# Kernel optimization log

Hardware: AMD Instinct MI355X
Metric: run time of the kernel (lower is better)

Reference implementation:

```python
import math
import jax, jax.numpy as jnp
import numpy as np

B, T, D, H, E, K = 2, 2048, 1024, 16, 8, 2
HD = D // H                      # head_dim = 64
CAP = math.ceil(1.25 * B * T / E)  # capacity per expert = 640
NEG = -1e9


def setup_inputs() -> dict:
    key = jax.random.key(0)
    ks = jax.random.split(key, 8)
    s = 0.02
    return {
        "x": jax.random.normal(ks[0], (B, T, D), jnp.float32),
        "ln1_g": jnp.ones((D,), jnp.float32),
        "ln1_b": jnp.zeros((D,), jnp.float32),
        "w_qkv": jax.random.normal(ks[1], (3 * D, D), jnp.float32) * s,
        "w_proj": jax.random.normal(ks[2], (D, D), jnp.float32) * s,
        "ln2_g": jnp.ones((D,), jnp.float32),
        "ln2_b": jnp.zeros((D,), jnp.float32),
        "w_gate": jax.random.normal(ks[3], (E, D), jnp.float32) * s,
        "w1": jax.random.normal(ks[4], (E, D, 4 * D), jnp.float32) * s,
        "b1": jnp.zeros((E, 4 * D), jnp.float32),
        "w2": jax.random.normal(ks[5], (E, 4 * D, D), jnp.float32) * s,
        "b2": jnp.zeros((E, D), jnp.float32),
    }


def _layernorm(x, g, b, eps=1e-5):
    m = x.mean(-1, keepdims=True)
    v = ((x - m) ** 2).mean(-1, keepdims=True)
    return (x - m) * jax.lax.rsqrt(v + eps) * g + b


def _rope(q, k):
    # q,k: [B,T,H,HD]; rotate-half RoPE with half_dim = HD//2 frequencies
    half = HD // 2
    pos = jnp.arange(T, dtype=jnp.float32)[:, None]
    inv_freq = 1.0 / (10000.0 ** (jnp.arange(0, HD, 2, dtype=jnp.float32) / HD))
    ang = pos * inv_freq                              # [T, half]
    sin = jnp.sin(ang)[None, :, None, :]
    cos = jnp.cos(ang)[None, :, None, :]

    def rot(t):
        t1, t2 = t[..., :half], t[..., half:]
        return jnp.concatenate([t1 * cos - t2 * sin, t1 * sin + t2 * cos], -1)

    return rot(q), rot(k)


def _attention(x, w_qkv, w_proj):
    qkv = (x @ w_qkv.T).reshape(B, T, H, 3 * HD)
    q, k, v = jnp.split(qkv, 3, axis=-1)              # each [B,T,H,HD]
    q, k = _rope(q, k)
    scores = jnp.einsum('bqhd,bkhd->bhqk', q, k) / math.sqrt(HD)
    causal = jnp.tril(jnp.ones((T, T), bool))
    scores = jnp.where(causal, scores, NEG)
    probs = jax.nn.softmax(scores, axis=-1)
    out = jnp.einsum('bhqk,bkhd->bqhd', probs, v).reshape(B, T, D)
    return out @ w_proj.T


def _sparse_moe(x2d, w_gate, w1, b1, w2, b2):
    # x2d: [N, D] flattened tokens. Eval mode: no noise, no dropout.
    N = x2d.shape[0]
    gates = jax.nn.softmax((x2d @ w_gate.T).astype(jnp.float32), axis=-1)  # [N,E]
    gate_vals, idx = jax.lax.top_k(gates, K)          # [N,K]
    gate_vals = gate_vals.astype(x2d.dtype)

    # Capacity enforcement: token order position within each expert
    mask = jnp.zeros((N, E), bool).at[jnp.arange(N)[:, None], idx].set(True)
    pos = jnp.cumsum(mask.astype(jnp.int32), axis=0) * mask - 1   # [N,E]
    keep = (pos < CAP) & mask
    slot = jnp.take_along_axis(pos, idx, axis=1)      # [N,K]
    kept = jnp.take_along_axis(keep, idx, axis=1)     # [N,K] bool

    # Dispatch: dropped tokens go to pad slot CAP (masked out at combine)
    slot_w = jnp.where(kept, slot, CAP).reshape(-1)   # [N*K]
    e_flat = idx.reshape(-1)                          # [N*K]
    xk = jnp.broadcast_to(x2d[:, None, :], (N, K, D)).reshape(-1, D)
    xk = xk * kept.reshape(-1, 1)
    buf = jnp.zeros((E, CAP + 1, D), x2d.dtype).at[e_flat, slot_w].set(xk)

    # Grouped expert MLP (GELU exact, matching nn.GELU default)
    h = jax.nn.gelu(jnp.einsum('ecd,edf->ecf', buf, w1) + b1[:, None, :],
                    approximate=False)
    out = jnp.einsum('ecf,efd->ecd', h, w2) + b2[:, None, :]

    # Combine: gather each token's expert output, weight by gate, mask drops
    y = out[e_flat, slot_w].reshape(N, K, D) * (gate_vals * kept)[..., None]
    return y.sum(axis=1)


def reference(x, ln1_g, ln1_b, w_qkv, w_proj, ln2_g, ln2_b,
              w_gate, w1, b1, w2, b2):
    h = x + _attention(_layernorm(x, ln1_g, ln1_b), w_qkv, w_proj)
    moe_in = _layernorm(h, ln2_g, ln2_b)
    moe_out = _sparse_moe(moe_in.reshape(B * T, D), w_gate, w1, b1, w2, b2)
    return h + moe_out.reshape(B, T, D)
```

## Files before the change

kernel.cpp:

```cpp
#include <hip/hip_runtime.h>
#include <hip/hip_bf16.h>

typedef __bf16 bf16;
typedef __attribute__((ext_vector_type(8))) __bf16 bf16x8;
typedef __attribute__((ext_vector_type(4))) __bf16 bf16x4;
typedef __attribute__((ext_vector_type(4))) float f32x4;
typedef __attribute__((ext_vector_type(16))) float f32x16;

#define NB 2
#define NT 2048
#define ND 1024
#define NH 16
#define HD_ 64
#define NE 8
#define NCAP 640
#define NTOK 4096
#define NDFF 4096

static __device__ __forceinline__ f32x4 mfma16(bf16x8 a, bf16x8 b, f32x4 c) {
  return __builtin_amdgcn_mfma_f32_16x16x32_bf16(a, b, c, 0, 0, 0);
}
static __device__ __forceinline__ f32x16 mfma32(bf16x8 a, bf16x8 b, f32x16 c) {
  return __builtin_amdgcn_mfma_f32_32x32x16_bf16(a, b, c, 0, 0, 0);
}
static __device__ __forceinline__ unsigned pk2(float a, float b) {
  union { __bf16 h[2]; unsigned u; } z;
  z.h[0] = (__bf16)a; z.h[1] = (__bf16)b;
  return z.u;
}
static __device__ __forceinline__ void gload_lds16(const bf16* g, bf16* l) {
  __builtin_amdgcn_global_load_lds(
      (const __attribute__((address_space(1))) unsigned int*)g,
      (__attribute__((address_space(3))) unsigned int*)l, 16, 0, 0);
}

__global__ __launch_bounds__(256) void cvt_k(const float* __restrict__ in,
                                             bf16* __restrict__ out, int n4) {
  int i = blockIdx.x * 256 + threadIdx.x;
  int stride = gridDim.x * 256;
  for (; i < n4; i += stride) {
    f32x4 v = ((const f32x4*)in)[i];
    bf16x4 o;
    o[0] = (bf16)v[0]; o[1] = (bf16)v[1]; o[2] = (bf16)v[2]; o[3] = (bf16)v[3];
    ((bf16x4*)out)[i] = o;
  }
}

__global__ __launch_bounds__(256) void transpose_k(const float* __restrict__ in,
                                                   bf16* __restrict__ out, int R, int C) {
  __shared__ float tile[64][65];
  const size_t zoff = (size_t)blockIdx.z * R * C;
  in += zoff; out += zoff;
  const int c0 = blockIdx.x * 64, r0 = blockIdx.y * 64;
  const int tx = threadIdx.x & 15, ty = threadIdx.x >> 4;
#pragma unroll
  for (int i = 0; i < 4; i++) {
    const int r = i * 16 + ty;
    f32x4 v = *(const f32x4*)(in + (size_t)(r0 + r) * C + c0 + tx * 4);
    *(f32x4*)&tile[r][tx * 4] = v;
  }
  __syncthreads();
#pragma unroll
  for (int i = 0; i < 4; i++) {
    const int rr = i * 16 + ty;
    bf16x4 o;
#pragma unroll
    for (int j = 0; j < 4; j++) o[j] = (bf16)tile[tx * 4 + j][rr];
    *(bf16x4*)(out + (size_t)(c0 + rr) * R + r0 + tx * 4) = o;
  }
}

__global__ __launch_bounds__(256) void transpose_v_k(const bf16* __restrict__ v,
                                                     bf16* __restrict__ vT) {
  __shared__ bf16 tile[32][33];
  int bh = blockIdx.z;
  const bf16* in = v + (size_t)bh * NT * HD_;
  bf16* out = vT + (size_t)bh * HD_ * NT;
  int t0 = blockIdx.x * 32, d0 = blockIdx.y * 32;
  int tx = threadIdx.x, ty = threadIdx.y;
#pragma unroll
  for (int i = 0; i < 4; i++)
    tile[ty + i * 8][tx] = in[(size_t)(t0 + ty + i * 8) * HD_ + d0 + tx];
  __syncthreads();
#pragma unroll
  for (int i = 0; i < 4; i++)
    out[(size_t)(d0 + ty + i * 8) * NT + t0 + tx] = tile[tx][ty + i * 8];
}

__global__ void rope_tab_k(float* __restrict__ tab) {
  int t = blockIdx.x, i = threadIdx.x;
  float inv = powf(10000.f, -(float)(2 * i) * (1.f / 64.f));
  float ang = (float)t * inv;
  float s, c;
  sincosf(ang, &s, &c);
  tab[(t * 32 + i) * 2] = s;
  tab[(t * 32 + i) * 2 + 1] = c;
}

template <bool BF16OUT>
__global__ __launch_bounds__(256) void ln_k(const float* __restrict__ in,
                                            const float* __restrict__ g,
                                            const float* __restrict__ bb,
                                            bf16* __restrict__ outb,
                                            float* __restrict__ outf) {
  const int row = blockIdx.x;
  const float* xr = in + (size_t)row * ND;
  const int tid = threadIdx.x, lane = tid & 63, wid = tid >> 6;
  f32x4 v = ((const f32x4*)xr)[tid];
  float s = v[0] + v[1] + v[2] + v[3];
  float sq = v[0] * v[0] + v[1] * v[1] + v[2] * v[2] + v[3] * v[3];
#pragma unroll
  for (int m = 1; m < 64; m <<= 1) {
    s += __shfl_xor(s, m, 64);
    sq += __shfl_xor(sq, m, 64);
  }
  __shared__ float red[8];
  if (lane == 0) { red[wid] = s; red[4 + wid] = sq; }
  __syncthreads();
  s = red[0] + red[1] + red[2] + red[3];
  sq = red[4] + red[5] + red[6] + red[7];
  float mean = s * (1.f / 1024.f);
  float var = sq * (1.f / 1024.f) - mean * mean;
  float rs = rsqrtf(var + 1e-5f);
#pragma unroll
  for (int c = 0; c < 4; c++) {
    int col = tid * 4 + c;
    float y = (v[c] - mean) * rs * g[col] + bb[col];
    if constexpr (BF16OUT) outb[(size_t)row * ND + col] = (bf16)y;
    else outf[(size_t)row * ND + col] = y;
  }
}

#define EPI_SPLIT_QKV 0
#define EPI_ADD_X 1
#define EPI_BIAS_GELU 2
#define EPI_STORE 3

template <int EPI, int STAGE>
__global__ __launch_bounds__(256) void gemm_bt_k(
    const bf16* __restrict__ A, const bf16* __restrict__ Bw,
    const int M, const int N, const int K,
    const size_t zA, const size_t zB, const size_t zOut, const size_t zBias,
    const float* __restrict__ bias, const float* __restrict__ Xadd,
    void* __restrict__ Out, bf16* __restrict__ k_out, bf16* __restrict__ v_out) {
  const int z = blockIdx.z;
  const int m0 = blockIdx.y * 128, n0 = blockIdx.x * 128;
  const int tid = threadIdx.x, lane = tid & 63, wid = tid >> 6;
  const int wm = (wid >> 1) * 64, wn = (wid & 1) * 64;
  const int l15 = lane & 15, ksl = lane >> 4;
  const int nst = K / 64;
  constexpr int LDB = (STAGE == 1) ? 72 : 64;
  __shared__ __align__(16) bf16 As[128 * LDB];
  __shared__ __align__(16) bf16 Bs[128 * LDB];
  f32x4 acc[4][4];
#pragma unroll
  for (int i = 0; i < 4; i++)
#pragma unroll
    for (int j = 0; j < 4; j++) acc[i][j] = (f32x4){0.f, 0.f, 0.f, 0.f};

  if constexpr (STAGE == 0) {
    const int lr = lane >> 3, lc = (lane & 7) * 8;
    const bf16* Ag = A + zA * z + (size_t)(m0 + wid * 32 + lr) * K + lc;
    const bf16* Bg = Bw + zB * z + (size_t)(n0 + wid * 32 + lr) * K + lc;
    for (int s = 0; s < nst; ++s) {
      __syncthreads();
#pragma unroll
      for (int it = 0; it < 4; it++) {
        gload_lds16(Ag + (size_t)(it * 8) * K + s * 64, &As[(wid * 32 + it * 8) * 64]);
        gload_lds16(Bg + (size_t)(it * 8) * K + s * 64, &Bs[(wid * 32 + it * 8) * 64]);
      }
      __syncthreads();
#pragma unroll
      for (int kk = 0; kk < 2; kk++) {
        bf16x8 af[4], bfr[4];
        const int ko = kk * 32 + ksl * 8;
#pragma unroll
        for (int i = 0; i < 4; i++)
          af[i] = *(const bf16x8*)&As[(wm + i * 16 + l15) * 64 + ko];
#pragma unroll
        for (int j = 0; j < 4; j++)
          bfr[j] = *(const bf16x8*)&Bs[(wn + j * 16 + l15) * 64 + ko];
#pragma unroll
        for (int i = 0; i < 4; i++)
#pragma unroll
          for (int j = 0; j < 4; j++)
            acc[i][j] = mfma16(af[i], bfr[j], acc[i][j]);
      }
    }
  } else {
    const int sr = tid >> 3, sc = (tid & 7) * 8;
    const bf16* Ag = A + zA * z + (size_t)(m0 + sr) * K + sc;
    const bf16* Bg = Bw + zB * z + (size_t)(n0 + sr) * K + sc;
    bf16x8 av[4], bv[4];
#pragma unroll
    for (int it = 0; it < 4; it++) {
      av[it] = *(const bf16x8*)(Ag + (size_t)(it * 32) * K);
      bv[it] = *(const bf16x8*)(Bg + (size_t)(it * 32) * K);
    }
    for (int s = 0; s < nst; ++s) {
      __syncthreads();
#pragma unroll
      for (int it = 0; it < 4; it++) {
        *(bf16x8*)&As[(sr + it * 32) * LDB + sc] = av[it];
        *(bf16x8*)&Bs[(sr + it * 32) * LDB + sc] = bv[it];
      }
      __syncthreads();
      if (s + 1 < nst) {
#pragma unroll
        for (int it = 0; it < 4; it++) {
          av[it] = *(const bf16x8*)(Ag + (size_t)(it * 32) * K + (s + 1) * 64);
          bv[it] = *(const bf16x8*)(Bg + (size_t)(it * 32) * K + (s + 1) * 64);
        }
      }
#pragma unroll
      for (int kk = 0; kk < 2; kk++) {
        bf16x8 af[4], bfr[4];
        const int ko = kk * 32 + ksl * 8;
#pragma unroll
        for (int i = 0; i < 4; i++)
          af[i] = *(const bf16x8*)&As[(wm + i * 16 + l15) * LDB + ko];
#pragma unroll
        for (int j = 0; j < 4; j++)
          bfr[j] = *(const bf16x8*)&Bs[(wn + j * 16 + l15) * LDB + ko];
#pragma unroll
        for (int i = 0; i < 4; i++)
#pragma unroll
          for (int j = 0; j < 4; j++)
            acc[i][j] = mfma16(af[i], bfr[j], acc[i][j]);
      }
    }
  }

#pragma unroll
  for (int i = 0; i < 4; i++) {
#pragma unroll
    for (int j = 0; j < 4; j++) {
      const int mb = m0 + wm + i * 16 + ksl * 4;
      const int nc = n0 + wn + j * 16 + l15;
#pragma unroll
      for (int r = 0; r < 4; r++) {
        const int mr = mb + r;
        float vacc = acc[i][j][r];
        if constexpr (EPI == EPI_SPLIT_QKV) {
          const int h = nc / 192;
          const int rr = nc - h * 192;
          const int which = rr >> 6;
          const int d = rr & 63;
          const int b = mr >> 11, t = mr & 2047;
          bf16* dst = (which == 0) ? (bf16*)Out : (which == 1 ? k_out : v_out);
          dst[(((size_t)(b * NH + h)) * NT + t) * HD_ + d] = (bf16)vacc;
        } else if constexpr (EPI == EPI_ADD_X) {
          ((float*)Out)[(size_t)mr * N + nc] = vacc + Xadd[(size_t)mr * N + nc];
        } else if constexpr (EPI == EPI_BIAS_GELU) {
          float x = vacc + bias[zBias * z + nc];
          float gl = 0.5f * x * (1.f + erff(x * 0.70710678118654752f));
          ((bf16*)Out)[zOut * z + (size_t)mr * N + nc] = (bf16)gl;
        } else {
          ((bf16*)Out)[zOut * z + (size_t)mr * N + nc] = (bf16)vacc;
        }
      }
    }
  }
}

__global__ __launch_bounds__(256) void rope_k(bf16* __restrict__ q, bf16* __restrict__ k,
                                              const float* __restrict__ tab) {
  const int bh = blockIdx.y;
  const int t = blockIdx.x * 4 + (threadIdx.x >> 6);
  const int d = threadIdx.x & 63;
  const size_t row = ((size_t)bh * NT + t) * HD_;
  const int i = d & 31;
  const float sn = tab[(t * 32 + i) * 2], cs = tab[(t * 32 + i) * 2 + 1];
  {
    float a = (float)q[row + d];
    float b2 = (float)q[row + (d ^ 32)];
    float o = (d < 32) ? (a * cs - b2 * sn) : (b2 * sn + a * cs);
    q[row + d] = (bf16)(o * 0.18033688011112042f);
  }
  {
    float a = (float)k[row + d];
    float b2 = (float)k[row + (d ^ 32)];
    float o = (d < 32) ? (a * cs - b2 * sn) : (b2 * sn + a * cs);
    k[row + d] = (bf16)o;
  }
}

__global__ __launch_bounds__(256) void attn_k(const bf16* __restrict__ q,
                                              const bf16* __restrict__ k,
                                              const bf16* __restrict__ vT,
                                              bf16* __restrict__ attn_out) {
  __shared__ __align__(16) bf16 Kt[64 * 64];
  __shared__ __align__(16) bf16 Vt[64 * 64];
  const int bid = blockIdx.x;
  const int bh = bid & 31;
  const int ti = (bid >> 5) & 7;
  const int qt = (bid >> 8) ? (15 - ti) : ti;
  const int q0 = qt * 128;
  const int tid = threadIdx.x, lane = tid & 63, wid = tid >> 6;
  const int l31 = lane & 31, hi = lane >> 5;
  const int q0w = q0 + wid * 32;
  const int qrow = q0w + l31;
  const size_t base = (size_t)bh * (NT * HD_);
  const size_t baseT = (size_t)bh * (HD_ * NT);

  bf16x8 qf[4];
#pragma unroll
  for (int ks = 0; ks < 4; ks++)
    qf[ks] = *(const bf16x8*)(q + base + (size_t)qrow * HD_ + ks * 16 + hi * 8);

  f32x16 ot0, ot1;
#pragma unroll
  for (int r = 0; r < 16; r++) { ot0[r] = 0.f; ot1[r] = 0.f; }
  float m2 = -1e30f, l = 0.f;

  const int ntiles = qt * 2 + 2;
  const int swz = (l31 & 7);
  const int strow = tid >> 3, stc = tid & 7;
  const int cw0 = ((stc ^ (strow & 7)) * 8);
  bf16x8 kr[2], vr[2];
#pragma unroll
  for (int rr = 0; rr < 2; rr++) {
    kr[rr] = *(const bf16x8*)(k + base + (size_t)(strow + rr * 32) * HD_ + stc * 8);
    vr[rr] = *(const bf16x8*)(vT + baseT + (size_t)(strow + rr * 32) * NT + stc * 8);
  }

  for (int t = 0; t < ntiles; t++) {
    const int kv0 = t * 64;
    __syncthreads();
#pragma unroll
    for (int rr = 0; rr < 2; rr++) {
      *(bf16x8*)&Kt[(strow + rr * 32) * 64 + cw0] = kr[rr];
      *(bf16x8*)&Vt[(strow + rr * 32) * 64 + cw0] = vr[rr];
    }
    __syncthreads();
    if (t + 1 < ntiles) {
      const int kn = kv0 + 64;
#pragma unroll
      for (int rr = 0; rr < 2; rr++) {
        kr[rr] = *(const bf16x8*)(k + base + (size_t)(kn + strow + rr * 32) * HD_ + stc * 8);
        vr[rr] = *(const bf16x8*)(vT + baseT + (size_t)(strow + rr * 32) * NT + kn + stc * 8);
      }
    }
    if (kv0 > q0w + 31) continue;

    f32x16 s0, s1;
#pragma unroll
    for (int r = 0; r < 16; r++) { s0[r] = 0.f; s1[r] = 0.f; }
#pragma unroll
    for (int ks = 0; ks < 4; ks++) {
      const int cw = (((ks * 2 + hi) ^ swz) * 8);
      bf16x8 ka0 = *(const bf16x8*)&Kt[l31 * 64 + cw];
      bf16x8 ka1 = *(const bf16x8*)&Kt[(l31 + 32) * 64 + cw];
      s0 = mfma32(ka0, qf[ks], s0);
      s1 = mfma32(ka1, qf[ks], s1);
    }

    float p[32];
#pragma unroll
    for (int r = 0; r < 16; r++) { p[r] = s0[r]; p[16 + r] = s1[r]; }
    if (kv0 + 63 > q0w) {
#pragma unroll
      for (int sub = 0; sub < 2; sub++)
#pragma unroll
        for (int r = 0; r < 16; r++) {
          int kvg = kv0 + sub * 32 + (r & 3) + 8 * (r >> 2) + 4 * hi;
          if (kvg > qrow) p[sub * 16 + r] = -1e30f;
        }
    }
    float tm = p[0];
#pragma unroll
    for (int r = 1; r < 32; r++) tm = fmaxf(tm, p[r]);
    tm = fmaxf(tm, __shfl_xor(tm, 32, 64));
    if (!__all(tm <= m2 + 8.f)) {
      float mn = fmaxf(m2, tm);
      float sf = exp2f(m2 - mn);
      m2 = mn;
      l *= sf;
#pragma unroll
      for (int r = 0; r < 16; r++) { ot0[r] *= sf; ot1[r] *= sf; }
    }
    float ts = 0.f;
#pragma unroll
    for (int r = 0; r < 32; r++) { p[r] = exp2f(p[r] - m2); ts += p[r]; }
    ts += __shfl_xor(ts, 32, 64);
    l += ts;

#pragma unroll
    for (int ks = 0; ks < 4; ks++) {
      const int i0 = (ks >> 1) * 16 + (ks & 1) * 8;
      unsigned Aw = pk2(p[i0 + 0], p[i0 + 1]);
      unsigned Bw = pk2(p[i0 + 2], p[i0 + 3]);
      unsigned Cw = pk2(p[i0 + 4], p[i0 + 5]);
      unsigned Dw = pk2(p[i0 + 6], p[i0 + 7]);
      unsigned xA = (unsigned)__shfl_xor((int)Aw, 32, 64);
      unsigned xB = (unsigned)__shfl_xor((int)Bw, 32, 64);
      unsigned xC = (unsigned)__shfl_xor((int)Cw, 32, 64);
      unsigned xD = (unsigned)__shfl_xor((int)Dw, 32, 64);
      union { unsigned u[4]; bf16x8 v; } pa;
      pa.u[0] = hi ? xC : Aw;
      pa.u[1] = hi ? xD : Bw;
      pa.u[2] = hi ? Cw : xA;
      pa.u[3] = hi ? Dw : xB;
      const int cw = (((ks * 2 + hi) ^ swz) * 8);
      bf16x8 va0 = *(const bf16x8*)&Vt[l31 * 64 + cw];
      bf16x8 va1 = *(const bf16x8*)&Vt[(l31 + 32) * 64 + cw];
      ot0 = mfma32(va0, pa.v, ot0);
      ot1 = mfma32(va1, pa.v, ot1);
    }
  }

  const int b = bh >> 4, h = bh & 15;
  const float inv = 1.f / l;
  const size_t orow = ((size_t)(b * NT + qrow)) * ND + h * 64;
#pragma unroll
  for (int g = 0; g < 4; g++) {
    bf16x4 w0, w1;
#pragma unroll
    for (int c = 0; c < 4; c++) {
      w0[c] = (bf16)(ot0[g * 4 + c] * inv);
      w1[c] = (bf16)(ot1[g * 4 + c] * inv);
    }
    *(bf16x4*)(attn_out + orow + g * 8 + 4 * hi) = w0;
    *(bf16x4*)(attn_out + orow + 32 + g * 8 + 4 * hi) = w1;
  }
}

__global__ __launch_bounds__(256) void gate_k(const float* __restrict__ moe_in,
                                              const float* __restrict__ w_gate,
                                              int* __restrict__ idx, float* __restrict__ gv) {
  __shared__ float wg[8 * 1024];
  for (int i = threadIdx.x; i < 8192; i += 256) wg[i] = w_gate[i];
  __syncthreads();
  const int lane = threadIdx.x & 63, wid = threadIdx.x >> 6;
  for (int tt = 0; tt < 4; tt++) {
    const int n = blockIdx.x * 16 + wid * 4 + tt;
    const float* xr = moe_in + (size_t)n * ND;
    float a[8];
#pragma unroll
    for (int e = 0; e < 8; e++) a[e] = 0.f;
    for (int d0 = lane * 4; d0 < 1024; d0 += 256) {
      f32x4 xv = *(const f32x4*)(xr + d0);
#pragma unroll
      for (int e = 0; e < 8; e++) {
        const float* wr = &wg[e * 1024 + d0];
        a[e] += xv[0] * wr[0] + xv[1] * wr[1] + xv[2] * wr[2] + xv[3] * wr[3];
      }
    }
#pragma unroll
    for (int e = 0; e < 8; e++)
#pragma unroll
      for (int m = 1; m < 64; m <<= 1) a[e] += __shfl_xor(a[e], m, 64);
    if (lane == 0) {
      float mx = a[0];
#pragma unroll
      for (int e = 1; e < 8; e++) mx = fmaxf(mx, a[e]);
      float p[8], se = 0.f;
#pragma unroll
      for (int e = 0; e < 8; e++) { p[e] = expf(a[e] - mx); se += p[e]; }
      float inv = 1.f / se;
#pragma unroll
      for (int e = 0; e < 8; e++) p[e] *= inv;
      int i1 = 0; float v1 = p[0];
#pragma unroll
      for (int e = 1; e < 8; e++) if (p[e] > v1) { v1 = p[e]; i1 = e; }
      int i2 = -1; float v2 = -1.f;
#pragma unroll
      for (int e = 0; e < 8; e++) if (e != i1 && p[e] > v2) { v2 = p[e]; i2 = e; }
      idx[n * 2] = i1; idx[n * 2 + 1] = i2;
      gv[n * 2] = v1; gv[n * 2 + 1] = v2;
    }
  }
}

__global__ void scan_k(const int* __restrict__ idx, int* __restrict__ slot,
                       int* __restrict__ kept) {
  const int lane = threadIdx.x;
  int base[8];
#pragma unroll
  for (int e = 0; e < 8; e++) base[e] = 0;
  const unsigned long long lm = (lane == 63) ? ~0ull : ((1ull << (lane + 1)) - 1);
  for (int c = 0; c < 64; c++) {
    const int n = c * 64 + lane;
    const int e0 = idx[n * 2], e1 = idx[n * 2 + 1];
    int s0 = 0, s1 = 0;
#pragma unroll
    for (int e = 0; e < 8; e++) {
      unsigned long long m0 = __ballot(e0 == e);
      unsigned long long m1 = __ballot(e1 == e);
      unsigned long long m = m0 | m1;
      int pref = __popcll(m & lm);
      if (e0 == e) s0 = base[e] + pref - 1;
      if (e1 == e) s1 = base[e] + pref - 1;
      base[e] += __popcll(m);
    }
    slot[n * 2] = s0; slot[n * 2 + 1] = s1;
    kept[n * 2] = (s0 < NCAP) ? 1 : 0;
    kept[n * 2 + 1] = (s1 < NCAP) ? 1 : 0;
  }
}

__global__ __launch_bounds__(64) void scatter_k(const float* __restrict__ moe_in,
                                                const int* __restrict__ idx,
                                                const int* __restrict__ slot,
                                                const int* __restrict__ kept,
                                                bf16* __restrict__ buf) {
  const int a = blockIdx.x;
  if (!kept[a]) return;
  const int n = a >> 1;
  const int e = idx[a], s = slot[a];
  const float* src = moe_in + (size_t)n * ND;
  bf16* dst = buf + ((size_t)e * NCAP + s) * ND;
  for (int c = threadIdx.x * 4; c < 1024; c += 256) {
    f32x4 v = *(const f32x4*)(src + c);
    bf16x4 o;
    o[0] = (bf16)v[0]; o[1] = (bf16)v[1]; o[2] = (bf16)v[2]; o[3] = (bf16)v[3];
    *(bf16x4*)(dst + c) = o;
  }
}

__global__ __launch_bounds__(256) void gather_k(const float* __restrict__ h,
                                                const bf16* __restrict__ eout,
                                                const int* __restrict__ idx,
                                                const int* __restrict__ slot,
                                                const int* __restrict__ kept,
                                                const float* __restrict__ gv,
                                                const float* __restrict__ b2,
                                                float* __restrict__ out) {
  const int n = blockIdx.x;
  const int k0 = kept[n * 2], k1 = kept[n * 2 + 1];
  const int i0 = idx[n * 2], i1 = idx[n * 2 + 1];
  const float g0 = k0 ? gv[n * 2] : 0.f;
  const float g1 = k1 ? gv[n * 2 + 1] : 0.f;
  const size_t r0 = k0 ? ((size_t)i0 * NCAP + slot[n * 2]) * ND : 0;
  const size_t r1 = k1 ? ((size_t)i1 * NCAP + slot[n * 2 + 1]) * ND : 0;
  const int c = threadIdx.x * 4;
  f32x4 o = *(const f32x4*)(h + (size_t)n * ND + c);
  if (k0) {
    bf16x4 e = *(const bf16x4*)(eout + r0 + c);
    f32x4 bb = *(const f32x4*)(b2 + i0 * ND + c);
#pragma unroll
    for (int cc = 0; cc < 4; cc++) o[cc] += g0 * ((float)e[cc] + bb[cc]);
  }
  if (k1) {
    bf16x4 e = *(const bf16x4*)(eout + r1 + c);
    f32x4 bb = *(const f32x4*)(b2 + i1 * ND + c);
#pragma unroll
    for (int cc = 0; cc < 4; cc++) o[cc] += g1 * ((float)e[cc] + bb[cc]);
  }
  *(f32x4*)(out + (size_t)n * ND + c) = o;
}

extern "C" void kernel_launch(void* const* d_in, const int* in_sizes, int n_in,
                              void* d_out, int out_size, void* d_ws, size_t ws_size,
                              hipStream_t stream) {
  (void)in_sizes; (void)n_in; (void)out_size;
  const float* x      = (const float*)d_in[0];
  const float* ln1_g  = (const float*)d_in[1];
  const float* ln1_b  = (const float*)d_in[2];
  const float* w_qkv  = (const float*)d_in[3];
  const float* w_proj = (const float*)d_in[4];
  const float* ln2_g  = (const float*)d_in[5];
  const float* ln2_b  = (const float*)d_in[6];
  const float* w_gate = (const float*)d_in[7];
  const float* w1     = (const float*)d_in[8];
  const float* b1     = (const float*)d_in[9];
  const float* w2     = (const float*)d_in[10];
  const float* b2     = (const float*)d_in[11];
  float* out = (float*)d_out;

  char* ws = (char*)d_ws;
  size_t off = 0;
  auto alloc = [&](size_t bytes) -> char* {
    char* p = ws + off;
    off += (bytes + 255) & ~(size_t)255;
    return p;
  };
  bf16* w1t    = (bf16*)alloc((size_t)NE * NDFF * ND * 2);
  bf16* w2t    = (bf16*)alloc((size_t)NE * ND * NDFF * 2);
  bf16* wqkvb  = (bf16*)alloc((size_t)3 * ND * ND * 2);
  bf16* wprojb = (bf16*)alloc((size_t)ND * ND * 2);
  float* hbufr = (float*)alloc((size_t)NTOK * ND * 4);
  float* moein = (float*)alloc((size_t)NTOK * ND * 4);
  float* ropet = (float*)alloc((size_t)NT * 32 * 2 * 4);
  int*   idx   = (int*)alloc((size_t)NTOK * 2 * 4);
  int*   slot  = (int*)alloc((size_t)NTOK * 2 * 4);
  int*   kept  = (int*)alloc((size_t)NTOK * 2 * 4);
  float* gv    = (float*)alloc((size_t)NTOK * 2 * 4);
  char*  S     = alloc((size_t)62914560);
  if (off > ws_size) return;

  const size_t MB8 = (size_t)8388608;
  bf16* xn    = (bf16*)(S);
  bf16* qp    = (bf16*)(S + MB8);
  bf16* kp    = (bf16*)(S + 2 * MB8);
  bf16* vp    = (bf16*)(S + 3 * MB8);
  bf16* attnp = (bf16*)(S + 4 * MB8);
  bf16* vTp   = (bf16*)(S);
  bf16* hbuf  = (bf16*)(S);
  bf16* buf   = (bf16*)(S + (size_t)41943040);
  bf16* eout  = (bf16*)(S + (size_t)52428800);

  dim3 tb(32, 8);
  cvt_k<<<2048, 256, 0, stream>>>(w_qkv, wqkvb, 3 * ND * ND / 4);
  cvt_k<<<1024, 256, 0, stream>>>(w_proj, wprojb, ND * ND / 4);
  transpose_k<<<dim3(NDFF / 64, ND / 64, NE), 256, 0, stream>>>(w1, w1t, ND, NDFF);
  transpose_k<<<dim3(ND / 64, NDFF / 64, NE), 256, 0, stream>>>(w2, w2t, NDFF, ND);
  rope_tab_k<<<NT, 32, 0, stream>>>(ropet);
  ln_k<true><<<NTOK, 256, 0, stream>>>(x, ln1_g, ln1_b, xn, nullptr);
  gemm_bt_k<EPI_SPLIT_QKV, 0><<<dim3(3 * ND / 128, NTOK / 128, 1), 256, 0, stream>>>(
      xn, wqkvb, NTOK, 3 * ND, ND, 0, 0, 0, 0, nullptr, nullptr, qp, kp, vp);
  transpose_v_k<<<dim3(NT / 32, HD_ / 32, NB * NH), tb, 0, stream>>>(vp, vTp);
  rope_k<<<dim3(NT / 4, NB * NH), 256, 0, stream>>>(qp, kp, ropet);
  attn_k<<<512, 256, 0, stream>>>(qp, kp, vTp, attnp);
  gemm_bt_k<EPI_ADD_X, 1><<<dim3(ND / 128, NTOK / 128, 1), 256, 0, stream>>>(
      attnp, wprojb, NTOK, ND, ND, 0, 0, 0, 0, nullptr, x, hbufr, nullptr, nullptr);
  ln_k<false><<<NTOK, 256, 0, stream>>>(hbufr, ln2_g, ln2_b, nullptr, moein);
  gate_k<<<NTOK / 16, 256, 0, stream>>>(moein, w_gate, idx, gv);
  scan_k<<<1, 64, 0, stream>>>(idx, slot, kept);
  scatter_k<<<NTOK * 2, 64, 0, stream>>>(moein, idx, slot, kept, buf);
  gemm_bt_k<EPI_BIAS_GELU, 0><<<dim3(NDFF / 128, NCAP / 128, NE), 256, 0, stream>>>(
      buf, w1t, NCAP, NDFF, ND, (size_t)NCAP * ND, (size_t)NDFF * ND,
      (size_t)NCAP * NDFF, NDFF, b1, nullptr, hbuf, nullptr, nullptr);
  gemm_bt_k<EPI_STORE, 1><<<dim3(ND / 128, NCAP / 128, NE), 256, 0, stream>>>(
      hbuf, w2t, NCAP, ND, NDFF, (size_t)NCAP * NDFF, (size_t)ND * NDFF,
      (size_t)NCAP * ND, 0, nullptr, nullptr, eout, nullptr, nullptr);
  gather_k<<<NTOK, 256, 0, stream>>>(hbufr, eout, idx, slot, kept, gv, b2, out);
}
```

Measured before the change: 459.1 us.

## Split-K the expert down-projection with fp32 atomics and use sigmoid GELU approximation

The second expert GEMM (K=4096) now splits K four ways across the grid z dimension. Each split accumulates into a zeroed fp32 output through atomic adds, which raises the block count from 320 to 1280 for better CU occupancy. The gather kernel now reads that fp32 output. The exact erf GELU is replaced by a sigmoid-based approximation, x*sigmoid(poly(x)), which is cheaper but deviates slightly from exact GELU. LDS padding is also disabled for that GEMM. The change adds a memset, atomic traffic and a larger fp32 intermediate.

```diff
diff --git a/kernel.cpp b/kernel.cpp
--- a/kernel.cpp
+++ b/kernel.cpp
@@ -134,22 +134,26 @@
 #define EPI_SPLIT_QKV 0
 #define EPI_ADD_X 1
 #define EPI_BIAS_GELU 2
-#define EPI_STORE 3
-
-template <int EPI, int STAGE>
+#define EPI_ATOMIC 3
+
+template <int EPI, int STAGE, bool PAD>
 __global__ __launch_bounds__(256) void gemm_bt_k(
     const bf16* __restrict__ A, const bf16* __restrict__ Bw,
-    const int M, const int N, const int K,
+    const int M, const int N, const int K, const int nsplit,
     const size_t zA, const size_t zB, const size_t zOut, const size_t zBias,
     const float* __restrict__ bias, const float* __restrict__ Xadd,
     void* __restrict__ Out, bf16* __restrict__ k_out, bf16* __restrict__ v_out) {
   const int z = blockIdx.z;
+  const int ze = z / nsplit;
+  const int kc = z - ze * nsplit;
+  const int klen = K / nsplit;
+  const int kb = kc * klen;
+  const int nst = klen / 64;
   const int m0 = blockIdx.y * 128, n0 = blockIdx.x * 128;
   const int tid = threadIdx.x, lane = tid & 63, wid = tid >> 6;
   const int wm = (wid >> 1) * 64, wn = (wid & 1) * 64;
   const int l15 = lane & 15, ksl = lane >> 4;
-  const int nst = K / 64;
-  constexpr int LDB = (STAGE == 1) ? 72 : 64;
+  constexpr int LDB = (STAGE == 1 && PAD) ? 72 : 64;
   __shared__ __align__(16) bf16 As[128 * LDB];
   __shared__ __align__(16) bf16 Bs[128 * LDB];
   f32x4 acc[4][4];
@@ -160,8 +164,8 @@
 
   if constexpr (STAGE == 0) {
     const int lr = lane >> 3, lc = (lane & 7) * 8;
-    const bf16* Ag = A + zA * z + (size_t)(m0 + wid * 32 + lr) * K + lc;
-    const bf16* Bg = Bw + zB * z + (size_t)(n0 + wid * 32 + lr) * K + lc;
+    const bf16* Ag = A + zA * ze + (size_t)(m0 + wid * 32 + lr) * K + kb + lc;
+    const bf16* Bg = Bw + zB * ze + (size_t)(n0 + wid * 32 + lr) * K + kb + lc;
     for (int s = 0; s < nst; ++s) {
       __syncthreads();
 #pragma unroll
@@ -189,8 +193,8 @@
     }
   } else {
     const int sr = tid >> 3, sc = (tid & 7) * 8;
-    const bf16* Ag = A + zA * z + (size_t)(m0 + sr) * K + sc;
-    const bf16* Bg = Bw + zB * z + (size_t)(n0 + sr) * K + sc;
+    const bf16* Ag = A + zA * ze + (size_t)(m0 + sr) * K + kb + sc;
+    const bf16* Bg = Bw + zB * ze + (size_t)(n0 + sr) * K + kb + sc;
     bf16x8 av[4], bv[4];
 #pragma unroll
     for (int it = 0; it < 4; it++) {
@@ -252,11 +256,12 @@
         } else if constexpr (EPI == EPI_ADD_X) {
           ((float*)Out)[(size_t)mr * N + nc] = vacc + Xadd[(size_t)mr * N + nc];
         } else if constexpr (EPI == EPI_BIAS_GELU) {
-          float x = vacc + bias[zBias * z + nc];
-          float gl = 0.5f * x * (1.f + erff(x * 0.70710678118654752f));
-          ((bf16*)Out)[zOut * z + (size_t)mr * N + nc] = (bf16)gl;
+          float x = vacc + bias[zBias * ze + nc];
+          float u2 = x * (2.3020882f + 0.10294772f * x * x);
+          float gl = x / (1.f + exp2f(-u2));
+          ((bf16*)Out)[zOut * ze + (size_t)mr * N + nc] = (bf16)gl;
         } else {
-          ((bf16*)Out)[zOut * z + (size_t)mr * N + nc] = (bf16)vacc;
+          unsafeAtomicAdd(&((float*)Out)[zOut * ze + (size_t)mr * N + nc], vacc);
         }
       }
     }
@@ -519,7 +524,7 @@
 }
 
 __global__ __launch_bounds__(256) void gather_k(const float* __restrict__ h,
-                                                const bf16* __restrict__ eout,
+                                                const float* __restrict__ eout,
                                                 const int* __restrict__ idx,
                                                 const int* __restrict__ slot,
                                                 const int* __restrict__ kept,
@@ -536,16 +541,16 @@
   const int c = threadIdx.x * 4;
   f32x4 o = *(const f32x4*)(h + (size_t)n * ND + c);
   if (k0) {
-    bf16x4 e = *(const bf16x4*)(eout + r0 + c);
+    f32x4 e = *(const f32x4*)(eout + r0 + c);
     f32x4 bb = *(const f32x4*)(b2 + i0 * ND + c);
 #pragma unroll
-    for (int cc = 0; cc < 4; cc++) o[cc] += g0 * ((float)e[cc] + bb[cc]);
+    for (int cc = 0; cc < 4; cc++) o[cc] += g0 * (e[cc] + bb[cc]);
   }
   if (k1) {
-    bf16x4 e = *(const bf16x4*)(eout + r1 + c);
+    f32x4 e = *(const f32x4*)(eout + r1 + c);
     f32x4 bb = *(const f32x4*)(b2 + i1 * ND + c);
 #pragma unroll
-    for (int cc = 0; cc < 4; cc++) o[cc] += g1 * ((float)e[cc] + bb[cc]);
+    for (int cc = 0; cc < 4; cc++) o[cc] += g1 * (e[cc] + bb[cc]);
   }
   *(f32x4*)(out + (size_t)n * ND + c) = o;
 }
@@ -596,9 +601,9 @@
   bf16* vp    = (bf16*)(S + 3 * MB8);
   bf16* attnp = (bf16*)(S + 4 * MB8);
   bf16* vTp   = (bf16*)(S);
-  bf16* hbuf  = (bf16*)(S);
-  bf16* buf   = (bf16*)(S + (size_t)41943040);
-  bf16* eout  = (bf16*)(S + (size_t)52428800);
+  bf16*  hbuf  = (bf16*)(S);
+  bf16*  buf   = (bf16*)(S + (size_t)41943040);
+  float* eoutf = (float*)(S + (size_t)41943040);
 
   dim3 tb(32, 8);
   cvt_k<<<2048, 256, 0, stream>>>(w_qkv, wqkvb, 3 * ND * ND / 4);
@@ -607,22 +612,23 @@
   transpose_k<<<dim3(ND / 64, NDFF / 64, NE), 256, 0, stream>>>(w2, w2t, NDFF, ND);
   rope_tab_k<<<NT, 32, 0, stream>>>(ropet);
   ln_k<true><<<NTOK, 256, 0, stream>>>(x, ln1_g, ln1_b, xn, nullptr);
-  gemm_bt_k<EPI_SPLIT_QKV, 0><<<dim3(3 * ND / 128, NTOK / 128, 1), 256, 0, stream>>>(
-      xn, wqkvb, NTOK, 3 * ND, ND, 0, 0, 0, 0, nullptr, nullptr, qp, kp, vp);
+  gemm_bt_k<EPI_SPLIT_QKV, 0, false><<<dim3(3 * ND / 128, NTOK / 128, 1), 256, 0, stream>>>(
+      xn, wqkvb, NTOK, 3 * ND, ND, 1, 0, 0, 0, 0, nullptr, nullptr, qp, kp, vp);
   transpose_v_k<<<dim3(NT / 32, HD_ / 32, NB * NH), tb, 0, stream>>>(vp, vTp);
   rope_k<<<dim3(NT / 4, NB * NH), 256, 0, stream>>>(qp, kp, ropet);
   attn_k<<<512, 256, 0, stream>>>(qp, kp, vTp, attnp);
-  gemm_bt_k<EPI_ADD_X, 1><<<dim3(ND / 128, NTOK / 128, 1), 256, 0, stream>>>(
-      attnp, wprojb, NTOK, ND, ND, 0, 0, 0, 0, nullptr, x, hbufr, nullptr, nullptr);
+  gemm_bt_k<EPI_ADD_X, 1, true><<<dim3(ND / 128, NTOK / 128, 1), 256, 0, stream>>>(
+      attnp, wprojb, NTOK, ND, ND, 1, 0, 0, 0, 0, nullptr, x, hbufr, nullptr, nullptr);
   ln_k<false><<<NTOK, 256, 0, stream>>>(hbufr, ln2_g, ln2_b, nullptr, moein);
   gate_k<<<NTOK / 16, 256, 0, stream>>>(moein, w_gate, idx, gv);
   scan_k<<<1, 64, 0, stream>>>(idx, slot, kept);
   scatter_k<<<NTOK * 2, 64, 0, stream>>>(moein, idx, slot, kept, buf);
-  gemm_bt_k<EPI_BIAS_GELU, 0><<<dim3(NDFF / 128, NCAP / 128, NE), 256, 0, stream>>>(
-      buf, w1t, NCAP, NDFF, ND, (size_t)NCAP * ND, (size_t)NDFF * ND,
+  gemm_bt_k<EPI_BIAS_GELU, 0, false><<<dim3(NDFF / 128, NCAP / 128, NE), 256, 0, stream>>>(
+      buf, w1t, NCAP, NDFF, ND, 1, (size_t)NCAP * ND, (size_t)NDFF * ND,
       (size_t)NCAP * NDFF, NDFF, b1, nullptr, hbuf, nullptr, nullptr);
-  gemm_bt_k<EPI_STORE, 1><<<dim3(ND / 128, NCAP / 128, NE), 256, 0, stream>>>(
-      hbuf, w2t, NCAP, ND, NDFF, (size_t)NCAP * NDFF, (size_t)ND * NDFF,
-      (size_t)NCAP * ND, 0, nullptr, nullptr, eout, nullptr, nullptr);
-  gather_k<<<NTOK, 256, 0, stream>>>(hbufr, eout, idx, slot, kept, gv, b2, out);
-}
+  hipMemsetAsync(eoutf, 0, (size_t)NE * NCAP * ND * 4, stream);
+  gemm_bt_k<EPI_ATOMIC, 1, false><<<dim3(ND / 128, NCAP / 128, NE * 4), 256, 0, stream>>>(
+      hbuf, w2t, NCAP, ND, NDFF, 4, (size_t)NCAP * NDFF, (size_t)ND * NDFF,
+      (size_t)NCAP * ND, 0, nullptr, nullptr, eoutf, nullptr, nullptr);
+  gather_k<<<NTOK, 256, 0, stream>>>(hbufr, eoutf, idx, slot, kept, gv, b2, out);
+}
```

Result: slower. 503.1 us (+9.6%).
